# Performance work log

Hardware: AMD Instinct MI355X
Metric: run time of the kernel (lower is better)

The kernel has to match this reference:

```python
import jax, jax.numpy as jnp
import numpy as np

NUM_HEADS = 8
HEAD_DIM = 64
D_MODEL = NUM_HEADS * HEAD_DIM  # 512
B, T = 4, 2048


def setup_inputs() -> dict:
    key = jax.random.key(0)
    k1, k2 = jax.random.split(key)
    x = jax.random.normal(k1, (B, T, D_MODEL), dtype=jnp.float32)
    mask = jnp.ones((B, 1, T, T), dtype=jnp.float32)
    W = jax.random.normal(k2, (D_MODEL, 3 * D_MODEL), dtype=jnp.float32) * (D_MODEL ** -0.5)
    b = jnp.zeros((3 * D_MODEL,), dtype=jnp.float32)
    return {"x": x, "mask": mask, "W": W, "b": b}


def reference(x, mask, W, b):
    batch = x.shape[0]
    # fused QKV projection: [B, T, 3D]
    qkv = jnp.einsum("btd,de->bte", x, W) + b
    # NOTE: faithful to torch reshape [B, T, H, Hd, 3] -> the size-3 axis is innermost
    qkv = qkv.reshape(batch, -1, NUM_HEADS, HEAD_DIM, 3)
    qkv = jnp.transpose(qkv, (4, 0, 2, 1, 3))  # [3, B, H, T, Hd]
    q, k, v = qkv[0], qkv[1], qkv[2]
    logits = jnp.einsum("bhqd,bhkd->bhqk", q, k) / (HEAD_DIM ** 0.5)
    logits = logits + (1.0 - mask) * -10000.0
    w = jax.nn.softmax(logits, axis=-1)
    out = jnp.einsum("bhqk,bhkd->bhqd", w, v)  # [B, H, T, Hd]
    out = jnp.transpose(out, (0, 2, 1, 3)).reshape(batch, -1, NUM_HEADS * HEAD_DIM)
    return out
```

## Files before the change

kernel.cpp:

```cpp
#include <hip/hip_runtime.h>
#include <hip/hip_bf16.h>
#include <stdint.h>

#define B_   4
#define T_   2048
#define H_   8
#define HD_  64
#define DM_  512
#define N3_  1536

typedef short bf_el;
typedef __attribute__((ext_vector_type(8))) bf_el bfrag;
typedef __attribute__((ext_vector_type(4))) float ffrag;

#define SCALE_L2E  0.18033688011112043f
#define MASK_L2E   14426.950408889634f

static __device__ __forceinline__ unsigned short f2bf(float f) {
    union { float f; unsigned int i; } v; v.f = f;
    unsigned int r = v.i + 0x7fff + ((v.i >> 16) & 1);
    return (unsigned short)(r >> 16);
}
static __device__ __forceinline__ unsigned short f2bf_fast(float f) {
    union { float f; unsigned int i; } v; v.f = f;
    return (unsigned short)((v.i + 0x8000u) >> 16);
}

__global__ __launch_bounds__(256) void k_prep(const float* __restrict__ W,
                                              const float* __restrict__ X,
                                              const float* __restrict__ mask,
                                              unsigned short* __restrict__ Wt,
                                              unsigned short* __restrict__ Xb,
                                              int* __restrict__ flags) {
    __shared__ __align__(16) unsigned short Ls[64 * 72];
    const int bid = blockIdx.x;
    const int tid = threadIdx.x;

    if (bid < 512) {
        const int R0 = bid * 16;
        const int mb = R0 >> 11;
        const int q0 = R0 & 2047;
        const int e  = mb * 32 + (q0 >> 6);
        const int wave = tid >> 6, lane = tid & 63;
        unsigned int acc = 0u;
        const float* base = mask + (size_t)R0 * T_ + tid * 8;
#pragma unroll
        for (int rr = 0; rr < 16; ++rr) {
            const uint4 u0 = *(const uint4*)(base + (size_t)rr * T_);
            const uint4 u1 = *(const uint4*)(base + (size_t)rr * T_ + 4);
            acc |= (u0.x ^ 0x3F800000u) | (u0.y ^ 0x3F800000u) |
                   (u0.z ^ 0x3F800000u) | (u0.w ^ 0x3F800000u) |
                   (u1.x ^ 0x3F800000u) | (u1.y ^ 0x3F800000u) |
                   (u1.z ^ 0x3F800000u) | (u1.w ^ 0x3F800000u);
        }
        unsigned long long bal = __ballot(acc != 0u);
        if (lane == 0 && bal != 0ULL) {
#pragma unroll
            for (int j = 0; j < 8; ++j)
                if ((bal >> (8 * j)) & 0xFFULL)
                    atomicOr(&flags[e * 32 + wave * 8 + j], 1);
        }
        return;
    }
    if (bid < 768) {
        const int b2 = bid - 512;
        const float* src = X + (size_t)b2 * 16384;
        unsigned short* dst = Xb + (size_t)b2 * 16384;
#pragma unroll
        for (int j = 0; j < 8; ++j) {
            int idx = j * 512 + tid * 2;
            float4 f0 = *(const float4*)(src + idx * 4);
            float4 f1 = *(const float4*)(src + idx * 4 + 4);
            __align__(16) unsigned short t8[8];
            t8[0] = f2bf_fast(f0.x); t8[1] = f2bf_fast(f0.y);
            t8[2] = f2bf_fast(f0.z); t8[3] = f2bf_fast(f0.w);
            t8[4] = f2bf_fast(f1.x); t8[5] = f2bf_fast(f1.y);
            t8[6] = f2bf_fast(f1.z); t8[7] = f2bf_fast(f1.w);
            *(uint4*)(dst + idx * 4) = *(const uint4*)t8;
        }
        return;
    }
    {
        const int t  = bid - 768;
        const int n0 = (t % 24) * 64;
        const int k0 = (t / 24) * 64;
#pragma unroll
        for (int i = 0; i < 4; ++i) {
            int chunk = tid + i * 256;
            int k = chunk >> 4;
            int c = chunk & 15;
            float4 f = *(const float4*)(W + (size_t)(k0 + k) * N3_ + n0 + c * 4);
            unsigned short* p = Ls + k * 72 + c * 4;
            p[0] = f2bf(f.x); p[1] = f2bf(f.y); p[2] = f2bf(f.z); p[3] = f2bf(f.w);
        }
        __syncthreads();
        const int n = tid >> 2;
        const int g = tid & 3;
        __align__(16) unsigned short tmp[16];
#pragma unroll
        for (int i = 0; i < 16; ++i) tmp[i] = Ls[(g * 16 + i) * 72 + n];
        uint4* dst = (uint4*)(Wt + (size_t)(n0 + n) * DM_ + k0 + g * 16);
        dst[0] = *(const uint4*)(tmp);
        dst[1] = *(const uint4*)(tmp + 8);
    }
}

__global__ __launch_bounds__(256) void k_gemm_qkv(const unsigned short* __restrict__ Xb,
                                                  const unsigned short* __restrict__ Wt,
                                                  const float* __restrict__ bias,
                                                  unsigned short* __restrict__ Qb,
                                                  unsigned short* __restrict__ Kb,
                                                  unsigned short* __restrict__ Vtb) {
    __shared__ __align__(16) unsigned short SH[12800];
    unsigned short* As = SH;
    unsigned short* Bs = SH + 5120;
    unsigned short* Cs = SH;

    const int tid  = threadIdx.x;
    const int wave = tid >> 6;
    const int lane = tid & 63;
    const int quad = lane >> 4;
    const int l16  = lane & 15;
    const int wm = wave >> 1, wn = wave & 1;
    const int h  = blockIdx.x >> 6;
    const int m0 = (blockIdx.x & 63) * 128;
    const int n0 = h * 192;

    float bvv[6];
#pragma unroll
    for (int ni = 0; ni < 6; ++ni) bvv[ni] = bias[n0 + wn * 96 + ni * 16 + l16];

    ffrag acc[4][6];
#pragma unroll
    for (int i = 0; i < 4; ++i)
#pragma unroll
        for (int j = 0; j < 6; ++j) acc[i][j] = (ffrag){0.f, 0.f, 0.f, 0.f};

    for (int kt = 0; kt < 16; ++kt) {
        __syncthreads();
#pragma unroll
        for (int i = 0; i < 2; ++i) {
            int chunk = tid + i * 256;
            int r = chunk >> 2, c = chunk & 3;
            *(uint4*)(As + r * 40 + c * 8) =
                *(const uint4*)(Xb + (size_t)(m0 + r) * DM_ + kt * 32 + c * 8);
        }
#pragma unroll
        for (int i = 0; i < 3; ++i) {
            int chunk = tid + i * 256;
            int r = chunk >> 2, c = chunk & 3;
            *(uint4*)(Bs + r * 40 + c * 8) =
                *(const uint4*)(Wt + (size_t)(n0 + r) * DM_ + kt * 32 + c * 8);
        }
        __syncthreads();
        bfrag af[4], bfr[6];
#pragma unroll
        for (int mi = 0; mi < 4; ++mi)
            af[mi] = *(const bfrag*)(As + (wm * 64 + mi * 16 + l16) * 40 + quad * 8);
#pragma unroll
        for (int ni = 0; ni < 6; ++ni)
            bfr[ni] = *(const bfrag*)(Bs + (wn * 96 + ni * 16 + l16) * 40 + quad * 8);
#pragma unroll
        for (int mi = 0; mi < 4; ++mi)
#pragma unroll
            for (int ni = 0; ni < 6; ++ni)
                acc[mi][ni] = __builtin_amdgcn_mfma_f32_16x16x32_bf16(af[mi], bfr[ni], acc[mi][ni], 0, 0, 0);
    }

    const int b   = m0 >> 11;
    const int tb0 = m0 & 2047;
    const size_t bh = (size_t)(b * 8 + h);
    float cscale[6];
#pragma unroll
    for (int ni = 0; ni < 6; ++ni) {
        int c = wn * 96 + ni * 16 + l16;
        cscale[ni] = (c % 3 == 0) ? SCALE_L2E : 1.0f;
    }
#pragma unroll
    for (int half = 0; half < 2; ++half) {
        __syncthreads();
        if (wm == half) {
#pragma unroll
            for (int mi = 0; mi < 4; ++mi)
#pragma unroll
                for (int ni = 0; ni < 6; ++ni)
#pragma unroll
                    for (int reg = 0; reg < 4; ++reg) {
                        int r = mi * 16 + quad * 4 + reg;
                        int c = wn * 96 + ni * 16 + l16;
                        Cs[r * 200 + c] = f2bf_fast((acc[mi][ni][reg] + bvv[ni]) * cscale[ni]);
                    }
        }
        __syncthreads();
        const int tb = tb0 + half * 64;
#pragma unroll
        for (int i = 0; i < 2; ++i) {
            int idx = tid + i * 256;
            int tl = idx >> 3, hc = (idx & 7) * 8;
            __align__(16) unsigned short tq[8], tk[8];
#pragma unroll
            for (int j = 0; j < 8; ++j) {
                tq[j] = Cs[tl * 200 + (hc + j) * 3 + 0];
                tk[j] = Cs[tl * 200 + (hc + j) * 3 + 1];
            }
            *(uint4*)(Qb + (bh * T_ + tb + tl) * HD_ + hc) = *(const uint4*)tq;
            *(uint4*)(Kb + (bh * T_ + tb + tl) * HD_ + hc) = *(const uint4*)tk;
        }
#pragma unroll
        for (int i = 0; i < 2; ++i) {
            int idx = tid + i * 256;
            int hd = idx >> 3, t8 = (idx & 7) * 8;
            __align__(16) unsigned short tv[8];
#pragma unroll
            for (int j = 0; j < 8; ++j)
                tv[j] = Cs[(t8 + j) * 200 + hd * 3 + 2];
            *(uint4*)(Vtb + (bh * HD_ + hd) * T_ + tb + t8) = *(const uint4*)tv;
        }
    }
}

__global__ __launch_bounds__(256) void k_attn(const unsigned short* __restrict__ Q,
                                              const unsigned short* __restrict__ K,
                                              const unsigned short* __restrict__ Vt,
                                              const float* __restrict__ mask,
                                              const int* __restrict__ flags,
                                              float* __restrict__ out) {
    __shared__ __align__(16) unsigned short Ks[2][64 * 72];
    __shared__ __align__(16) unsigned short Vs[2][64 * 72];
    __shared__ __align__(16) unsigned short Ps[4][16 * 72];

    const int tid = threadIdx.x;
    const int wave = tid >> 6, lane = tid & 63;
    const int quad = lane >> 4, l16 = lane & 15;
    const int bh = blockIdx.x & 31, b = bh >> 3, h = bh & 7;
    const int qt = blockIdx.x >> 5;
    const int q0 = qt * 128;

    bfrag qf[2][2];
#pragma unroll
    for (int g = 0; g < 2; ++g) {
        size_t qrow = ((size_t)bh * T_ + q0 + wave * 32 + g * 16 + l16) * HD_;
        qf[g][0] = *(const bfrag*)(Q + qrow + quad * 8);
        qf[g][1] = *(const bfrag*)(Q + qrow + 32 + quad * 8);
    }
    float lsum[2][4] = {{0.f,0.f,0.f,0.f},{0.f,0.f,0.f,0.f}};
    ffrag of[2][4];
#pragma unroll
    for (int g = 0; g < 2; ++g)
#pragma unroll
        for (int nb = 0; nb < 4; ++nb) of[g][nb] = (ffrag){0.f, 0.f, 0.f, 0.f};

    const int fbase0 = (b * 32 + qt * 2) * 32;
    const int fbase1 = (b * 32 + qt * 2 + 1) * 32;

    const int sr0 = tid >> 3, sr1 = (tid + 256) >> 3, sc = tid & 7;
    const unsigned short* Kbase = K  + (size_t)bh * T_ * HD_;
    const unsigned short* Vbase = Vt + (size_t)bh * HD_ * T_;

    uint4 kreg[2], vreg[2];
    kreg[0] = *(const uint4*)(Kbase + (size_t)sr0 * HD_ + sc * 8);
    kreg[1] = *(const uint4*)(Kbase + (size_t)sr1 * HD_ + sc * 8);
    vreg[0] = *(const uint4*)(Vbase + (size_t)sr0 * T_ + sc * 8);
    vreg[1] = *(const uint4*)(Vbase + (size_t)sr1 * T_ + sc * 8);
    *(uint4*)(&Ks[0][sr0 * 72 + sc * 8]) = kreg[0];
    *(uint4*)(&Ks[0][sr1 * 72 + sc * 8]) = kreg[1];
    *(uint4*)(&Vs[0][sr0 * 72 + sc * 8]) = vreg[0];
    *(uint4*)(&Vs[0][sr1 * 72 + sc * 8]) = vreg[1];
    __syncthreads();

    for (int kt = 0; kt < 32; ++kt) {
        const int cur = kt & 1;
        if (kt < 31) {
            const int kn = (kt + 1) * 64;
            kreg[0] = *(const uint4*)(Kbase + (size_t)(kn + sr0) * HD_ + sc * 8);
            kreg[1] = *(const uint4*)(Kbase + (size_t)(kn + sr1) * HD_ + sc * 8);
            vreg[0] = *(const uint4*)(Vbase + (size_t)sr0 * T_ + kn + sc * 8);
            vreg[1] = *(const uint4*)(Vbase + (size_t)sr1 * T_ + kn + sc * 8);
        }
        int fl[2];
        fl[0] = flags[fbase0 + kt];
        fl[1] = flags[fbase1 + kt];

        bfrag vf[2][4];
#pragma unroll
        for (int ks = 0; ks < 2; ++ks)
#pragma unroll
            for (int nb = 0; nb < 4; ++nb)
                vf[ks][nb] = *(const bfrag*)(&Vs[cur][(nb * 16 + l16) * 72 + (ks * 4 + quad) * 8]);

#pragma unroll
        for (int g = 0; g < 2; ++g) {
            ffrag sf[4];
#pragma unroll
            for (int ns = 0; ns < 4; ++ns) {
                ffrag a = (ffrag){0.f, 0.f, 0.f, 0.f};
#pragma unroll
                for (int ks = 0; ks < 2; ++ks) {
                    bfrag kf = *(const bfrag*)(&Ks[cur][(ns * 16 + l16) * 72 + (ks * 4 + quad) * 8]);
                    a = __builtin_amdgcn_mfma_f32_16x16x32_bf16(qf[g][ks], kf, a, 0, 0, 0);
                }
                sf[ns] = a;
            }
            if (fl[g]) {
#pragma unroll
                for (int reg = 0; reg < 4; ++reg) {
                    int tq = q0 + wave * 32 + g * 16 + quad * 4 + reg;
                    const float* mrow = mask + ((size_t)b * T_ + tq) * T_ + kt * 64;
#pragma unroll
                    for (int ns = 0; ns < 4; ++ns) {
                        float msk = mrow[ns * 16 + l16];
                        float p = __builtin_amdgcn_exp2f(
                            fmaf(msk, MASK_L2E, sf[ns][reg] - MASK_L2E));
                        lsum[g][reg] += p;
                        Ps[wave][(quad * 4 + reg) * 72 + ns * 16 + l16] = f2bf_fast(p);
                    }
                }
            } else {
#pragma unroll
                for (int reg = 0; reg < 4; ++reg) {
#pragma unroll
                    for (int ns = 0; ns < 4; ++ns) {
                        float p = __builtin_amdgcn_exp2f(sf[ns][reg]);
                        lsum[g][reg] += p;
                        Ps[wave][(quad * 4 + reg) * 72 + ns * 16 + l16] = f2bf_fast(p);
                    }
                }
            }
#pragma unroll
            for (int ks = 0; ks < 2; ++ks) {
                bfrag pf = *(const bfrag*)(&Ps[wave][l16 * 72 + (ks * 4 + quad) * 8]);
#pragma unroll
                for (int nb = 0; nb < 4; ++nb)
                    of[g][nb] = __builtin_amdgcn_mfma_f32_16x16x32_bf16(pf, vf[ks][nb], of[g][nb], 0, 0, 0);
            }
        }
        if (kt < 31) {
            const int nxt = cur ^ 1;
            *(uint4*)(&Ks[nxt][sr0 * 72 + sc * 8]) = kreg[0];
            *(uint4*)(&Ks[nxt][sr1 * 72 + sc * 8]) = kreg[1];
            *(uint4*)(&Vs[nxt][sr0 * 72 + sc * 8]) = vreg[0];
            *(uint4*)(&Vs[nxt][sr1 * 72 + sc * 8]) = vreg[1];
            __syncthreads();
        }
    }
#pragma unroll
    for (int g = 0; g < 2; ++g)
#pragma unroll
    for (int reg = 0; reg < 4; ++reg) {
        float s = lsum[g][reg];
#pragma unroll
        for (int d = 1; d < 16; d <<= 1) s += __shfl_xor(s, d, 64);
        float inv = 1.0f / s;
        int t = q0 + wave * 32 + g * 16 + quad * 4 + reg;
#pragma unroll
        for (int nb = 0; nb < 4; ++nb)
            out[((size_t)b * T_ + t) * DM_ + h * 64 + nb * 16 + l16] = of[g][nb][reg] * inv;
    }
}

extern "C" void kernel_launch(void* const* d_in, const int* in_sizes, int n_in,
                              void* d_out, int out_size, void* d_ws, size_t ws_size,
                              hipStream_t stream) {
    const float* X    = (const float*)d_in[0];
    const float* mask = (const float*)d_in[1];
    const float* W    = (const float*)d_in[2];
    const float* bias = (const float*)d_in[3];
    float* outp = (float*)d_out;

    char* ws = (char*)d_ws;
    unsigned short* Wt  = (unsigned short*)(ws);
    unsigned short* Xb  = (unsigned short*)(ws + 1572864);
    unsigned short* Qb  = (unsigned short*)(ws + 9961472);
    unsigned short* Kb  = (unsigned short*)(ws + 18350080);
    unsigned short* Vtb = (unsigned short*)(ws + 26738688);
    int*            flg = (int*)(ws + 35127296);

    hipMemsetAsync(flg, 0, 16384, stream);
    k_prep     <<<dim3(960), 256, 0, stream>>>(W, X, mask, Wt, Xb, flg);
    k_gemm_qkv <<<dim3(512), 256, 0, stream>>>(Xb, Wt, bias, Qb, Kb, Vtb);
    k_attn     <<<dim3(512), 256, 0, stream>>>(Qb, Kb, Vtb, mask, flg, outp);
}
```

Measured before the change: 216.4 us.

## Split attention key tiles across wave pairs and keep P in registers

Reworks the attention kernel so each pair of waves covers 64 query rows and each wave handles half of every 64-key tile. QK^T is computed transposed (K as the A operand), so the softmax probabilities land directly in the register layout the PV MFMA needs. This removes the per-wave LDS staging buffer for P and packs pairs of values with v_cvt_pk_bf16. Partial outputs and row sums from the two key halves are combined through LDS at the end. Mask loads become float4 vectors, and launch bounds ask for 2 blocks per SM, at the cost of more accumulator registers and an extra reduction step.

```diff
diff --git a/kernel.cpp b/kernel.cpp
--- a/kernel.cpp
+++ b/kernel.cpp
@@ -11,6 +11,7 @@
 
 typedef short bf_el;
 typedef __attribute__((ext_vector_type(8))) bf_el bfrag;
+typedef __attribute__((ext_vector_type(4))) bf_el bhalf4;
 typedef __attribute__((ext_vector_type(4))) float ffrag;
 
 #define SCALE_L2E  0.18033688011112043f
@@ -24,6 +25,12 @@
 static __device__ __forceinline__ unsigned short f2bf_fast(float f) {
     union { float f; unsigned int i; } v; v.f = f;
     return (unsigned short)((v.i + 0x8000u) >> 16);
+}
+
+static __device__ __forceinline__ unsigned int cvt_pk_bf16(float a, float b) {
+    unsigned int r;
+    asm("v_cvt_pk_bf16_f32 %0, %1, %2" : "=v"(r) : "v"(a), "v"(b));
+    return r;
 }
 
 __global__ __launch_bounds__(256) void k_prep(const float* __restrict__ W,
@@ -219,39 +226,39 @@
     }
 }
 
-__global__ __launch_bounds__(256) void k_attn(const unsigned short* __restrict__ Q,
-                                              const unsigned short* __restrict__ K,
-                                              const unsigned short* __restrict__ Vt,
-                                              const float* __restrict__ mask,
-                                              const int* __restrict__ flags,
-                                              float* __restrict__ out) {
-    __shared__ __align__(16) unsigned short Ks[2][64 * 72];
-    __shared__ __align__(16) unsigned short Vs[2][64 * 72];
-    __shared__ __align__(16) unsigned short Ps[4][16 * 72];
+__global__ __launch_bounds__(256, 2) void k_attn(const unsigned short* __restrict__ Q,
+                                                 const unsigned short* __restrict__ K,
+                                                 const unsigned short* __restrict__ Vt,
+                                                 const float* __restrict__ mask,
+                                                 const int* __restrict__ flags,
+                                                 float* __restrict__ out) {
+    __shared__ __align__(16) unsigned short KVs[4][64 * 72];
+    __shared__ float Rs[256];
 
     const int tid = threadIdx.x;
     const int wave = tid >> 6, lane = tid & 63;
     const int quad = lane >> 4, l16 = lane & 15;
+    const int rg = wave & 1;
+    const int kh = wave >> 1;
     const int bh = blockIdx.x & 31, b = bh >> 3, h = bh & 7;
     const int qt = blockIdx.x >> 5;
     const int q0 = qt * 128;
 
-    bfrag qf[2][2];
-#pragma unroll
-    for (int g = 0; g < 2; ++g) {
-        size_t qrow = ((size_t)bh * T_ + q0 + wave * 32 + g * 16 + l16) * HD_;
+    bfrag qf[4][2];
+#pragma unroll
+    for (int g = 0; g < 4; ++g) {
+        size_t qrow = ((size_t)bh * T_ + q0 + rg * 64 + g * 16 + l16) * HD_;
         qf[g][0] = *(const bfrag*)(Q + qrow + quad * 8);
         qf[g][1] = *(const bfrag*)(Q + qrow + 32 + quad * 8);
     }
-    float lsum[2][4] = {{0.f,0.f,0.f,0.f},{0.f,0.f,0.f,0.f}};
-    ffrag of[2][4];
-#pragma unroll
-    for (int g = 0; g < 2; ++g)
+    float lsum[4] = {0.f, 0.f, 0.f, 0.f};
+    ffrag of[4][4];
+#pragma unroll
+    for (int g = 0; g < 4; ++g)
 #pragma unroll
         for (int nb = 0; nb < 4; ++nb) of[g][nb] = (ffrag){0.f, 0.f, 0.f, 0.f};
 
-    const int fbase0 = (b * 32 + qt * 2) * 32;
-    const int fbase1 = (b * 32 + qt * 2 + 1) * 32;
+    const int fbase = (b * 32 + qt * 2 + rg) * 32;
 
     const int sr0 = tid >> 3, sr1 = (tid + 256) >> 3, sc = tid & 7;
     const unsigned short* Kbase = K  + (size_t)bh * T_ * HD_;
@@ -262,10 +269,10 @@
     kreg[1] = *(const uint4*)(Kbase + (size_t)sr1 * HD_ + sc * 8);
     vreg[0] = *(const uint4*)(Vbase + (size_t)sr0 * T_ + sc * 8);
     vreg[1] = *(const uint4*)(Vbase + (size_t)sr1 * T_ + sc * 8);
-    *(uint4*)(&Ks[0][sr0 * 72 + sc * 8]) = kreg[0];
-    *(uint4*)(&Ks[0][sr1 * 72 + sc * 8]) = kreg[1];
-    *(uint4*)(&Vs[0][sr0 * 72 + sc * 8]) = vreg[0];
-    *(uint4*)(&Vs[0][sr1 * 72 + sc * 8]) = vreg[1];
+    *(uint4*)(&KVs[0][sr0 * 72 + sc * 8]) = kreg[0];
+    *(uint4*)(&KVs[0][sr1 * 72 + sc * 8]) = kreg[1];
+    *(uint4*)(&KVs[2][sr0 * 72 + sc * 8]) = vreg[0];
+    *(uint4*)(&KVs[2][sr1 * 72 + sc * 8]) = vreg[1];
     __syncthreads();
 
     for (int kt = 0; kt < 32; ++kt) {
@@ -277,84 +284,125 @@
             vreg[0] = *(const uint4*)(Vbase + (size_t)sr0 * T_ + kn + sc * 8);
             vreg[1] = *(const uint4*)(Vbase + (size_t)sr1 * T_ + kn + sc * 8);
         }
-        int fl[2];
-        fl[0] = flags[fbase0 + kt];
-        fl[1] = flags[fbase1 + kt];
-
-        bfrag vf[2][4];
-#pragma unroll
-        for (int ks = 0; ks < 2; ++ks)
-#pragma unroll
-            for (int nb = 0; nb < 4; ++nb)
-                vf[ks][nb] = *(const bfrag*)(&Vs[cur][(nb * 16 + l16) * 72 + (ks * 4 + quad) * 8]);
-
-#pragma unroll
-        for (int g = 0; g < 2; ++g) {
-            ffrag sf[4];
-#pragma unroll
-            for (int ns = 0; ns < 4; ++ns) {
+        const int fl = flags[fbase + kt];
+
+        bfrag kf[2][2];
+#pragma unroll
+        for (int ns = 0; ns < 2; ++ns) {
+            const int nsg = kh * 2 + ns;
+#pragma unroll
+            for (int ks = 0; ks < 2; ++ks)
+                kf[ns][ks] = *(const bfrag*)(&KVs[cur][(nsg * 16 + l16) * 72 + (ks * 4 + quad) * 8]);
+        }
+        bfrag vfr[4];
+#pragma unroll
+        for (int nb = 0; nb < 4; ++nb) {
+            union { bhalf4 h[2]; bfrag f; } vv;
+            vv.h[0] = *(const bhalf4*)(&KVs[2 + cur][(nb * 16 + l16) * 72 + kh * 32 + quad * 4]);
+            vv.h[1] = *(const bhalf4*)(&KVs[2 + cur][(nb * 16 + l16) * 72 + kh * 32 + 16 + quad * 4]);
+            vfr[nb] = vv.f;
+        }
+
+#pragma unroll
+        for (int g = 0; g < 4; ++g) {
+            ffrag st[2];
+#pragma unroll
+            for (int ns = 0; ns < 2; ++ns) {
                 ffrag a = (ffrag){0.f, 0.f, 0.f, 0.f};
-#pragma unroll
-                for (int ks = 0; ks < 2; ++ks) {
-                    bfrag kf = *(const bfrag*)(&Ks[cur][(ns * 16 + l16) * 72 + (ks * 4 + quad) * 8]);
-                    a = __builtin_amdgcn_mfma_f32_16x16x32_bf16(qf[g][ks], kf, a, 0, 0, 0);
-                }
-                sf[ns] = a;
+                a = __builtin_amdgcn_mfma_f32_16x16x32_bf16(kf[ns][0], qf[g][0], a, 0, 0, 0);
+                a = __builtin_amdgcn_mfma_f32_16x16x32_bf16(kf[ns][1], qf[g][1], a, 0, 0, 0);
+                st[ns] = a;
             }
-            if (fl[g]) {
-#pragma unroll
-                for (int reg = 0; reg < 4; ++reg) {
-                    int tq = q0 + wave * 32 + g * 16 + quad * 4 + reg;
-                    const float* mrow = mask + ((size_t)b * T_ + tq) * T_ + kt * 64;
-#pragma unroll
-                    for (int ns = 0; ns < 4; ++ns) {
-                        float msk = mrow[ns * 16 + l16];
-                        float p = __builtin_amdgcn_exp2f(
-                            fmaf(msk, MASK_L2E, sf[ns][reg] - MASK_L2E));
-                        lsum[g][reg] += p;
-                        Ps[wave][(quad * 4 + reg) * 72 + ns * 16 + l16] = f2bf_fast(p);
+            float p[2][4];
+            if (fl) {
+                const float* mrow = mask + ((size_t)b * T_ + q0 + rg * 64 + g * 16 + l16) * T_
+                                  + kt * 64 + kh * 32 + quad * 4;
+#pragma unroll
+                for (int ns = 0; ns < 2; ++ns) {
+                    float mv[4];
+                    *(float4*)mv = *(const float4*)(mrow + ns * 16);
+#pragma unroll
+                    for (int reg = 0; reg < 4; ++reg) {
+                        float pv = __builtin_amdgcn_exp2f(
+                            fmaf(mv[reg], MASK_L2E, st[ns][reg] - MASK_L2E));
+                        p[ns][reg] = pv;
+                        lsum[g] += pv;
                     }
                 }
             } else {
 #pragma unroll
-                for (int reg = 0; reg < 4; ++reg) {
-#pragma unroll
-                    for (int ns = 0; ns < 4; ++ns) {
-                        float p = __builtin_amdgcn_exp2f(sf[ns][reg]);
-                        lsum[g][reg] += p;
-                        Ps[wave][(quad * 4 + reg) * 72 + ns * 16 + l16] = f2bf_fast(p);
+                for (int ns = 0; ns < 2; ++ns)
+#pragma unroll
+                    for (int reg = 0; reg < 4; ++reg) {
+                        float pv = __builtin_amdgcn_exp2f(st[ns][reg]);
+                        p[ns][reg] = pv;
+                        lsum[g] += pv;
                     }
-                }
             }
-#pragma unroll
-            for (int ks = 0; ks < 2; ++ks) {
-                bfrag pf = *(const bfrag*)(&Ps[wave][l16 * 72 + (ks * 4 + quad) * 8]);
-#pragma unroll
-                for (int nb = 0; nb < 4; ++nb)
-                    of[g][nb] = __builtin_amdgcn_mfma_f32_16x16x32_bf16(pf, vf[ks][nb], of[g][nb], 0, 0, 0);
-            }
+            union { unsigned int u[4]; bfrag s; } pa;
+            pa.u[0] = cvt_pk_bf16(p[0][0], p[0][1]);
+            pa.u[1] = cvt_pk_bf16(p[0][2], p[0][3]);
+            pa.u[2] = cvt_pk_bf16(p[1][0], p[1][1]);
+            pa.u[3] = cvt_pk_bf16(p[1][2], p[1][3]);
+#pragma unroll
+            for (int nb = 0; nb < 4; ++nb)
+                of[g][nb] = __builtin_amdgcn_mfma_f32_16x16x32_bf16(pa.s, vfr[nb], of[g][nb], 0, 0, 0);
         }
         if (kt < 31) {
             const int nxt = cur ^ 1;
-            *(uint4*)(&Ks[nxt][sr0 * 72 + sc * 8]) = kreg[0];
-            *(uint4*)(&Ks[nxt][sr1 * 72 + sc * 8]) = kreg[1];
-            *(uint4*)(&Vs[nxt][sr0 * 72 + sc * 8]) = vreg[0];
-            *(uint4*)(&Vs[nxt][sr1 * 72 + sc * 8]) = vreg[1];
+            *(uint4*)(&KVs[nxt][sr0 * 72 + sc * 8]) = kreg[0];
+            *(uint4*)(&KVs[nxt][sr1 * 72 + sc * 8]) = kreg[1];
+            *(uint4*)(&KVs[2 + nxt][sr0 * 72 + sc * 8]) = vreg[0];
+            *(uint4*)(&KVs[2 + nxt][sr1 * 72 + sc * 8]) = vreg[1];
             __syncthreads();
         }
     }
-#pragma unroll
-    for (int g = 0; g < 2; ++g)
-#pragma unroll
-    for (int reg = 0; reg < 4; ++reg) {
-        float s = lsum[g][reg];
-#pragma unroll
-        for (int d = 1; d < 16; d <<= 1) s += __shfl_xor(s, d, 64);
-        float inv = 1.0f / s;
-        int t = q0 + wave * 32 + g * 16 + quad * 4 + reg;
-#pragma unroll
-        for (int nb = 0; nb < 4; ++nb)
-            out[((size_t)b * T_ + t) * DM_ + h * 64 + nb * 16 + l16] = of[g][nb][reg] * inv;
+
+    float rsw[4];
+#pragma unroll
+    for (int g = 0; g < 4; ++g) {
+        float r = lsum[g];
+        r += __shfl_xor(r, 16, 64);
+        r += __shfl_xor(r, 32, 64);
+        rsw[g] = r;
+    }
+    __syncthreads();
+    float* Fp = (float*)(&KVs[0][0]);
+    if (quad == 0) {
+#pragma unroll
+        for (int g = 0; g < 4; ++g)
+            Rs[kh * 128 + rg * 64 + g * 16 + l16] = rsw[g];
+    }
+    if (kh == 1) {
+        float* basep = Fp + rg * (64 * 66);
+#pragma unroll
+        for (int g = 0; g < 4; ++g)
+#pragma unroll
+            for (int nb = 0; nb < 4; ++nb)
+#pragma unroll
+                for (int reg = 0; reg < 4; ++reg)
+                    basep[(g * 16 + quad * 4 + reg) * 66 + nb * 16 + l16] = of[g][nb][reg];
+    }
+    __syncthreads();
+    if (kh == 0) {
+        const float* basep = Fp + rg * (64 * 66);
+#pragma unroll
+        for (int g = 0; g < 4; ++g) {
+            float inv[4];
+#pragma unroll
+            for (int reg = 0; reg < 4; ++reg) {
+                int row = rg * 64 + g * 16 + quad * 4 + reg;
+                inv[reg] = 1.0f / (Rs[row] + Rs[128 + row]);
+            }
+#pragma unroll
+            for (int nb = 0; nb < 4; ++nb)
+#pragma unroll
+                for (int reg = 0; reg < 4; ++reg) {
+                    float v = of[g][nb][reg] + basep[(g * 16 + quad * 4 + reg) * 66 + nb * 16 + l16];
+                    int t = q0 + rg * 64 + g * 16 + quad * 4 + reg;
+                    out[((size_t)b * T_ + t) * DM_ + h * 64 + nb * 16 + l16] = v * inv[reg];
+                }
+        }
     }
 }
 
```

Measured after the change: 197.7 us. 1.09x faster.
